# Optimization experiments

Hardware: AMD Instinct MI355X
Metric: run time of the kernel (lower is better)

Reference implementation:

```python
import jax
import jax.numpy as jnp
import numpy as np

B, S, D, H, HID, E, TOPK = 1, 2048, 1024, 16, 4096, 8, 2
HEAD_DIM = D // H


def _layer_norm(x, g, b, eps=1e-5):
    mu = jnp.mean(x, axis=-1, keepdims=True)
    var = jnp.var(x, axis=-1, keepdims=True)
    return (x - mu) * jax.lax.rsqrt(var + eps) * g + b


def setup_inputs() -> dict:
    key = jax.random.key(0)
    ks = jax.random.split(key, 12)
    s = 0.02
    return {
        "x": jax.random.normal(ks[0], (B, S, D), jnp.float32),
        "ln1_g": jnp.ones((D,), jnp.float32),
        "ln1_b": jnp.zeros((D,), jnp.float32),
        "wq": jax.random.normal(ks[1], (D, D), jnp.float32) * s,
        "wk": jax.random.normal(ks[2], (D, D), jnp.float32) * s,
        "wv": jax.random.normal(ks[3], (D, D), jnp.float32) * s,
        "wo": jax.random.normal(ks[4], (D, D), jnp.float32) * s,
        "ln2_g": jnp.ones((D,), jnp.float32),
        "ln2_b": jnp.zeros((D,), jnp.float32),
        "w_gate": jax.random.normal(ks[5], (D, E), jnp.float32) * s,
        "w_eg": jax.random.normal(ks[6], (E, D, HID), jnp.float32) * s,
        "w_eu": jax.random.normal(ks[7], (E, D, HID), jnp.float32) * s,
        "w_ed": jax.random.normal(ks[8], (E, HID, D), jnp.float32) * s,
    }


def _attention(h, wq, wk, wv, wo):
    b, s, d = h.shape
    q = (h @ wq).reshape(b, s, H, HEAD_DIM).transpose(0, 2, 1, 3)
    k = (h @ wk).reshape(b, s, H, HEAD_DIM).transpose(0, 2, 1, 3)
    v = (h @ wv).reshape(b, s, H, HEAD_DIM).transpose(0, 2, 1, 3)
    scores = jnp.einsum("bhqd,bhkd->bhqk", q, k) / jnp.sqrt(jnp.asarray(HEAD_DIM, h.dtype))
    causal = jnp.tril(jnp.ones((s, s), bool))  # [s,s]
    scores = jnp.where(causal, scores, jnp.asarray(-1e30, h.dtype))
    attn = jax.nn.softmax(scores, axis=-1)
    out = jnp.einsum("bhqk,bhkd->bhqd", attn, v).transpose(0, 2, 1, 3).reshape(b, s, d)
    return out @ wo


def _moe(h, w_gate, w_eg, w_eu, w_ed):
    b, s, d = h.shape
    flat = h.reshape(-1, d)  # [T,D]
    logits = flat @ w_gate  # [T,E]
    scores = jax.nn.sigmoid(logits)
    top_val, top_idx = jax.lax.top_k(scores, TOPK)
    top_val = top_val / (jnp.sum(top_val, axis=-1, keepdims=True) + 1e-9)
    # per-token per-expert combine weight (0 for unrouted experts)
    combine = jnp.sum(jax.nn.one_hot(top_idx, E, dtype=flat.dtype) * top_val[..., None], axis=1)  # [T,E]
    g = jax.nn.silu(jnp.einsum("td,edh->eth", flat, w_eg))
    u = jnp.einsum("td,edh->eth", flat, w_eu)
    eo = jnp.einsum("eth,ehd->etd", g * u, w_ed)  # [E,T,D]
    out = jnp.einsum("etd,te->td", eo, combine)
    return out.reshape(b, s, d)


def reference(x, ln1_g, ln1_b, wq, wk, wv, wo, ln2_g, ln2_b, w_gate, w_eg, w_eu, w_ed):
    x = x + _attention(_layer_norm(x, ln1_g, ln1_b), wq, wk, wv, wo)
    x = x + _moe(_layer_norm(x, ln2_g, ln2_b), w_gate, w_eg, w_eu, w_ed)
    return x
```

## Files before the change

kernel.cpp:

```cpp
#include <hip/hip_runtime.h>
#include <hip/hip_bf16.h>
#include <stdint.h>

#define DI __device__ __forceinline__

typedef short bf16x8_t __attribute__((ext_vector_type(8)));
typedef float f32x4_t __attribute__((ext_vector_type(4)));

DI unsigned short f2bf(float f) {
  __hip_bfloat16 h = __float2bfloat16(f);
  unsigned short u;
  __builtin_memcpy(&u, &h, 2);
  return u;
}

DI uint32_t pk2(float a, float b) {
  return (uint32_t)f2bf(a) | ((uint32_t)f2bf(b) << 16);
}

DI f32x4_t mfma16(bf16x8_t a, bf16x8_t b, f32x4_t c) {
  return __builtin_amdgcn_mfma_f32_16x16x32_bf16(a, b, c, 0, 0, 0);
}

DI void gload16(const void* g, void* l) {
  __builtin_amdgcn_global_load_lds(
      (const __attribute__((address_space(1))) uint32_t*)g,
      (__attribute__((address_space(3))) uint32_t*)l, 16, 0, 0);
}

DI bf16x8_t frag(const unsigned short* base, int row, int hi) {
  return *(const bf16x8_t*)&base[row * 32 + ((hi ^ ((row >> 1) & 3)) * 8)];
}
DI int chunk_swz(int tid) { return ((tid & 3) ^ ((tid >> 3) & 3)) * 8; }

__global__ __launch_bounds__(256) void transpose_cvt(const float* __restrict__ in,
                                                     unsigned short* __restrict__ out,
                                                     int R, int C) {
  __shared__ float tile[64][65];
  const int tid = threadIdx.x;
  const int tx = tid & 15, ty = tid >> 4;
  const size_t zoff = (size_t)blockIdx.z * R * C;
  const int r0 = blockIdx.y * 64, c0 = blockIdx.x * 64;
#pragma unroll
  for (int i = 0; i < 4; ++i) {
    const int r = ty + i * 16;
    const float4 v = *(const float4*)(in + zoff + (size_t)(r0 + r) * C + c0 + tx * 4);
    tile[r][tx * 4 + 0] = v.x; tile[r][tx * 4 + 1] = v.y;
    tile[r][tx * 4 + 2] = v.z; tile[r][tx * 4 + 3] = v.w;
  }
  __syncthreads();
#pragma unroll
  for (int i = 0; i < 4; ++i) {
    const int r = ty + i * 16;
    ushort4 o;
    o.x = f2bf(tile[tx * 4 + 0][r]); o.y = f2bf(tile[tx * 4 + 1][r]);
    o.z = f2bf(tile[tx * 4 + 2][r]); o.w = f2bf(tile[tx * 4 + 3][r]);
    *(ushort4*)(out + zoff + (size_t)(c0 + r) * R + r0 + tx * 4) = o;
  }
}

__global__ __launch_bounds__(256) void ln_kernel(const float* __restrict__ x, const float* __restrict__ g,
                                                 const float* __restrict__ b, unsigned short* __restrict__ out) {
  const int row = blockIdx.x, tid = threadIdx.x;
  const int wid = tid >> 6, lane = tid & 63;
  const float4 v = *(const float4*)(x + (size_t)row * 1024 + tid * 4);
  float s = v.x + v.y + v.z + v.w;
  float s2 = v.x * v.x + v.y * v.y + v.z * v.z + v.w * v.w;
#pragma unroll
  for (int o = 1; o < 64; o <<= 1) { s += __shfl_xor(s, o); s2 += __shfl_xor(s2, o); }
  __shared__ float red[8];
  if (lane == 0) { red[wid] = s; red[4 + wid] = s2; }
  __syncthreads();
  const float ts = red[0] + red[1] + red[2] + red[3];
  const float ts2 = red[4] + red[5] + red[6] + red[7];
  const float mu = ts * 0.0009765625f;
  const float var = ts2 * 0.0009765625f - mu * mu;
  const float rs = rsqrtf(var + 1e-5f);
  const float4 gg = *(const float4*)(g + tid * 4);
  const float4 bb = *(const float4*)(b + tid * 4);
  ushort4 o4;
  o4.x = f2bf((v.x - mu) * rs * gg.x + bb.x);
  o4.y = f2bf((v.y - mu) * rs * gg.y + bb.y);
  o4.z = f2bf((v.z - mu) * rs * gg.z + bb.z);
  o4.w = f2bf((v.w - mu) * rs * gg.w + bb.w);
  *(ushort4*)(out + (size_t)row * 1024 + tid * 4) = o4;
}

template<int BN>
DI void gemm_loop(const unsigned short* aR0, const unsigned short* aR1,
                  const unsigned short* bR0, const unsigned short* bR1,
                  const int K, unsigned short* lds, const int tid,
                  f32x4_t (&acc)[4][BN / 32]) {
  constexpr int NF = BN / 32;
  unsigned short* ldsA = lds;
  unsigned short* ldsB = lds + 4096;
  const int wid = tid >> 6, lane = tid & 63, ln = lane & 15, hi = lane >> 4;
  const int wr = wid >> 1, wc = wid & 1;
  char* dstA0 = (char*)ldsA + wid * 1024;
  char* dstA1 = (char*)ldsA + 4096 + wid * 1024;
  char* dstB0 = (char*)ldsB + wid * 1024;
  char* dstB1 = (char*)ldsB + 4096 + wid * 1024;
  for (int k0 = 0; k0 < K; k0 += 32) {
    gload16(aR0 + k0, dstA0);
    gload16(aR1 + k0, dstA1);
    gload16(bR0 + k0, dstB0);
    if constexpr (BN == 128) gload16(bR1 + k0, dstB1);
    __syncthreads();
    bf16x8_t af[4];
#pragma unroll
    for (int mf = 0; mf < 4; ++mf)
      af[mf] = frag(ldsA, wr * 64 + mf * 16 + ln, hi);
#pragma unroll
    for (int nf = 0; nf < NF; ++nf) {
      bf16x8_t bfr = frag(ldsB, wc * (BN / 2) + nf * 16 + ln, hi);
#pragma unroll
      for (int mf = 0; mf < 4; ++mf)
        acc[mf][nf] = mfma16(af[mf], bfr, acc[mf][nf]);
    }
    __syncthreads();
  }
}

__global__ __launch_bounds__(256) void qkv_kernel(const unsigned short* __restrict__ h1,
                                                  const unsigned short* __restrict__ wqT,
                                                  const unsigned short* __restrict__ wkT,
                                                  const unsigned short* __restrict__ wvT,
                                                  unsigned short* __restrict__ qb,
                                                  unsigned short* __restrict__ kbf,
                                                  unsigned short* __restrict__ vt) {
  __shared__ unsigned short lds[128 * 32 + 128 * 32];
  const int tid = threadIdx.x;
  const int z = blockIdx.z;
  const unsigned short* BT = (z == 0) ? wqT : (z == 1) ? wkT : wvT;
  const int m0 = blockIdx.y * 128, n0 = blockIdx.x * 128;
  f32x4_t acc[4][4] = {};
  const int cs = chunk_swz(tid);
  const unsigned short* aR0 = h1 + (size_t)(m0 + (tid >> 2)) * 1024 + cs;
  const unsigned short* aR1 = aR0 + 64 * 1024;
  const unsigned short* bR0 = BT + (size_t)(n0 + (tid >> 2)) * 1024 + cs;
  const unsigned short* bR1 = bR0 + 64 * 1024;
  gemm_loop<128>(aR0, aR1, bR0, bR1, 1024, lds, tid, acc);
  const int lane = tid & 63, ln = lane & 15, hi = lane >> 4, wid = tid >> 6;
  const int wr = wid >> 1, wc = wid & 1;
  if (z < 2) {
    unsigned short* o = z ? kbf : qb;
#pragma unroll
    for (int mf = 0; mf < 4; ++mf)
#pragma unroll
      for (int nf = 0; nf < 4; ++nf)
#pragma unroll
        for (int r = 0; r < 4; ++r) {
          const int m = m0 + wr * 64 + mf * 16 + hi * 4 + r;
          const int n = n0 + wc * 64 + nf * 16 + ln;
          o[(size_t)m * 1024 + n] = f2bf(acc[mf][nf][r]);
        }
  } else {
#pragma unroll
    for (int mf = 0; mf < 4; ++mf)
#pragma unroll
      for (int nf = 0; nf < 4; ++nf) {
        const int n = n0 + wc * 64 + nf * 16 + ln;
        const int mb = m0 + wr * 64 + mf * 16 + hi * 4;
        ushort4 o;
        o.x = f2bf(acc[mf][nf][0]); o.y = f2bf(acc[mf][nf][1]);
        o.z = f2bf(acc[mf][nf][2]); o.w = f2bf(acc[mf][nf][3]);
        *(ushort4*)(vt + (size_t)n * 2048 + mb) = o;
      }
  }
}

__global__ __launch_bounds__(256) void wo_kernel(const unsigned short* __restrict__ ao,
                                                 const unsigned short* __restrict__ woT,
                                                 const float* __restrict__ x,
                                                 float* __restrict__ out) {
  __shared__ unsigned short lds[128 * 32 + 64 * 32];
  const int tid = threadIdx.x;
  const int m0 = blockIdx.y * 128, n0 = blockIdx.x * 64;
  f32x4_t acc[4][2] = {};
  const int cs = chunk_swz(tid);
  const unsigned short* aR0 = ao + (size_t)(m0 + (tid >> 2)) * 1024 + cs;
  const unsigned short* aR1 = aR0 + 64 * 1024;
  const unsigned short* bR0 = woT + (size_t)(n0 + (tid >> 2)) * 1024 + cs;
  gemm_loop<64>(aR0, aR1, bR0, nullptr, 1024, lds, tid, acc);
  const int lane = tid & 63, ln = lane & 15, hi = lane >> 4, wid = tid >> 6;
  const int wr = wid >> 1, wc = wid & 1;
#pragma unroll
  for (int mf = 0; mf < 4; ++mf)
#pragma unroll
    for (int nf = 0; nf < 2; ++nf)
#pragma unroll
      for (int r = 0; r < 4; ++r) {
        const int m = m0 + wr * 64 + mf * 16 + hi * 4 + r;
        const int n = n0 + wc * 32 + nf * 16 + ln;
        out[(size_t)m * 1024 + n] = acc[mf][nf][r] + x[(size_t)m * 1024 + n];
      }
}

__global__ __launch_bounds__(256) void attn_kernel(const unsigned short* __restrict__ qb,
                                                   const unsigned short* __restrict__ kbuf,
                                                   const unsigned short* __restrict__ vt,
                                                   unsigned short* __restrict__ ao) {
  __shared__ unsigned short kTl[4096];
  __shared__ unsigned short vTl[4096];
  __shared__ unsigned short pl[4][1024];
  const int tid = threadIdx.x;
  const int wid = tid >> 6, lane = tid & 63;
  const int ln = lane & 15, hi = lane >> 4;
  const int h = blockIdx.y;
  const int q0 = blockIdx.x * 64;
  const int q0w = q0 + wid * 16;

  const unsigned short* qrow = qb + (size_t)(q0w + ln) * 1024 + h * 64 + hi * 8;
  const bf16x8_t aq0 = *(const bf16x8_t*)(qrow);
  const bf16x8_t aq1 = *(const bf16x8_t*)(qrow + 32);

  const int str_r = tid >> 3, str_c = tid & 7;
  const int swc = (str_c ^ (str_r & 7)) * 8;
  const unsigned short* ksrc0 = kbuf + (size_t)str_r * 1024 + h * 64 + swc;
  const unsigned short* ksrc1 = kbuf + (size_t)(str_r + 32) * 1024 + h * 64 + swc;
  const unsigned short* vsrc0 = vt + (size_t)(h * 64 + str_r) * 2048 + swc;
  const unsigned short* vsrc1 = vt + (size_t)(h * 64 + str_r + 32) * 2048 + swc;
  char* kd0 = (char*)kTl + wid * 1024;
  char* kd1 = (char*)kTl + 4096 + wid * 1024;
  char* vd0 = (char*)vTl + wid * 1024;
  char* vd1 = (char*)vTl + 4096 + wid * 1024;

  float m_r[4], l_r[4];
  f32x4_t o_acc[4] = {};
#pragma unroll
  for (int r = 0; r < 4; ++r) { m_r[r] = -1e30f; l_r[r] = 0.f; }

  const int nkv = blockIdx.x + 1;
  for (int it = 0; it < nkv; ++it) {
    const int kv0 = it * 64;
    gload16(ksrc0 + (size_t)kv0 * 1024, kd0);
    gload16(ksrc1 + (size_t)kv0 * 1024, kd1);
    gload16(vsrc0 + kv0, vd0);
    gload16(vsrc1 + kv0, vd1);
    __syncthreads();

    float sc[4][4];
#pragma unroll
    for (int cf = 0; cf < 4; ++cf) {
      const int row = cf * 16 + ln;
      const int swz = row & 7;
      const bf16x8_t b0 = *(const bf16x8_t*)((char*)kTl + row * 128 + ((hi ^ swz) * 16));
      const bf16x8_t b1 = *(const bf16x8_t*)((char*)kTl + row * 128 + (((4 + hi) ^ swz) * 16));
      f32x4_t zacc = {};
      zacc = mfma16(aq0, b0, zacc);
      zacc = mfma16(aq1, b1, zacc);
#pragma unroll
      for (int r = 0; r < 4; ++r) sc[cf][r] = zacc[r] * 0.125f;
    }
    if (kv0 + 63 > q0w) {
#pragma unroll
      for (int cf = 0; cf < 4; ++cf)
#pragma unroll
        for (int r = 0; r < 4; ++r) {
          const int qg = q0w + hi * 4 + r;
          const int kg = kv0 + cf * 16 + ln;
          if (kg > qg) sc[cf][r] = -1e30f;
        }
    }
#pragma unroll
    for (int r = 0; r < 4; ++r) {
      float tm = fmaxf(fmaxf(sc[0][r], sc[1][r]), fmaxf(sc[2][r], sc[3][r]));
      tm = fmaxf(tm, __shfl_xor(tm, 1));
      tm = fmaxf(tm, __shfl_xor(tm, 2));
      tm = fmaxf(tm, __shfl_xor(tm, 4));
      tm = fmaxf(tm, __shfl_xor(tm, 8));
      const float mn = fmaxf(m_r[r], tm);
      const float alpha = __expf(m_r[r] - mn);
      float rsum = 0.f;
#pragma unroll
      for (int cf = 0; cf < 4; ++cf) {
        const float p = __expf(sc[cf][r] - mn);
        sc[cf][r] = p; rsum += p;
      }
      rsum += __shfl_xor(rsum, 1); rsum += __shfl_xor(rsum, 2);
      rsum += __shfl_xor(rsum, 4); rsum += __shfl_xor(rsum, 8);
      l_r[r] = l_r[r] * alpha + rsum;
      m_r[r] = mn;
#pragma unroll
      for (int df = 0; df < 4; ++df) o_acc[df][r] *= alpha;
    }
    unsigned short* pw = &pl[wid][0];
#pragma unroll
    for (int cf = 0; cf < 4; ++cf)
#pragma unroll
      for (int r = 0; r < 4; ++r) {
        const int qq = hi * 4 + r;
        const int kv = cf * 16 + ln;
        const int bo = (qq * 128 + kv * 2) ^ ((qq & 7) << 4);
        *(unsigned short*)((char*)pw + bo) = f2bf(sc[cf][r]);
      }
    __syncthreads();
    const bf16x8_t pa0 = *(const bf16x8_t*)((char*)pw + ((ln * 128 + hi * 16) ^ ((ln & 7) << 4)));
    const bf16x8_t pa1 = *(const bf16x8_t*)((char*)pw + ((ln * 128 + 64 + hi * 16) ^ ((ln & 7) << 4)));
#pragma unroll
    for (int df = 0; df < 4; ++df) {
      const int d = df * 16 + ln;
      const int swz = d & 7;
      const bf16x8_t bv0 = *(const bf16x8_t*)((char*)vTl + d * 128 + ((hi ^ swz) * 16));
      const bf16x8_t bv1 = *(const bf16x8_t*)((char*)vTl + d * 128 + (((4 + hi) ^ swz) * 16));
      o_acc[df] = mfma16(pa0, bv0, o_acc[df]);
      o_acc[df] = mfma16(pa1, bv1, o_acc[df]);
    }
    __syncthreads();
  }
#pragma unroll
  for (int df = 0; df < 4; ++df) {
    const int n = h * 64 + df * 16 + ln;
#pragma unroll
    for (int r = 0; r < 4; ++r) {
      const int m = q0w + hi * 4 + r;
      ao[(size_t)m * 1024 + n] = f2bf(o_acc[df][r] / l_r[r]);
    }
  }
}

__global__ __launch_bounds__(256) void gate_kernel(const float* __restrict__ x2, const float* __restrict__ g,
                                                   const float* __restrict__ b, const float* __restrict__ wg,
                                                   int2* __restrict__ te, float2* __restrict__ tw,
                                                   int* __restrict__ cnt) {
  const int tid = threadIdx.x, wid = tid >> 6, lane = tid & 63;
  const int t = blockIdx.x * 4 + wid;
  const float* row = x2 + (size_t)t * 1024;
  float vv[16];
#pragma unroll
  for (int i = 0; i < 4; ++i) *(float4*)&vv[i * 4] = *(const float4*)(row + lane * 16 + i * 4);
  float s = 0.f, s2 = 0.f;
#pragma unroll
  for (int j = 0; j < 16; ++j) { s += vv[j]; s2 += vv[j] * vv[j]; }
#pragma unroll
  for (int o = 1; o < 64; o <<= 1) { s += __shfl_xor(s, o); s2 += __shfl_xor(s2, o); }
  const float mu = s * 0.0009765625f;
  const float var = s2 * 0.0009765625f - mu * mu;
  const float rs = rsqrtf(var + 1e-5f);
  float acc[8] = {0.f, 0.f, 0.f, 0.f, 0.f, 0.f, 0.f, 0.f};
#pragma unroll
  for (int j = 0; j < 16; ++j) {
    const int d = lane * 16 + j;
    const float xv = (vv[j] - mu) * rs * g[d] + b[d];
    const float4 w0 = *(const float4*)(wg + d * 8);
    const float4 w1 = *(const float4*)(wg + d * 8 + 4);
    acc[0] += xv * w0.x; acc[1] += xv * w0.y; acc[2] += xv * w0.z; acc[3] += xv * w0.w;
    acc[4] += xv * w1.x; acc[5] += xv * w1.y; acc[6] += xv * w1.z; acc[7] += xv * w1.w;
  }
#pragma unroll
  for (int o = 1; o < 64; o <<= 1) {
#pragma unroll
    for (int e = 0; e < 8; ++e) acc[e] += __shfl_xor(acc[e], o);
  }
  if (lane == 0) {
    float sg[8];
#pragma unroll
    for (int e = 0; e < 8; ++e) sg[e] = 1.f / (1.f + __expf(-acc[e]));
    int e0 = 0;
#pragma unroll
    for (int e = 1; e < 8; ++e) if (sg[e] > sg[e0]) e0 = e;
    int e1 = (e0 == 0) ? 1 : 0;
#pragma unroll
    for (int e = 0; e < 8; ++e) if (e != e0 && sg[e] > sg[e1]) e1 = e;
    const float v0 = sg[e0], v1 = sg[e1];
    const float inv = 1.f / (v0 + v1 + 1e-9f);
    te[t] = make_int2(e0, e1);
    tw[t] = make_float2(v0 * inv, v1 * inv);
    atomicAdd(&cnt[e0], 1);
    atomicAdd(&cnt[e1], 1);
  }
}

__global__ void zero_counters(int* p) { if (threadIdx.x < 8) p[threadIdx.x] = 0; }

__global__ void g2_kernel(const int* __restrict__ cnt, int* __restrict__ slot_off,
                          int* __restrict__ tile_expert, int* __restrict__ tile_rowbase,
                          int* __restrict__ cursor, int* __restrict__ assign_token,
                          float* __restrict__ assign_w) {
  const int tid = threadIdx.x;
  for (int i = tid; i < 5120; i += 64) { assign_token[i] = -1; assign_w[i] = 0.f; }
  if (tid == 0) {
    int base = 0, tiles = 0;
    for (int e = 0; e < 8; ++e) {
      const int c = cnt[e];
      slot_off[e] = base;
      cursor[e] = 0;
      const int nt = (c + 127) >> 7;
      for (int i = 0; i < nt; ++i) {
        tile_expert[tiles] = e;
        tile_rowbase[tiles] = base + i * 128;
        ++tiles;
      }
      base += nt * 128;
    }
    for (; tiles < 40; ++tiles) tile_expert[tiles] = -1;
  }
}

__global__ __launch_bounds__(256) void g3_kernel(const int2* __restrict__ te, const float2* __restrict__ tw,
                                                 const int* __restrict__ slot_off, int* __restrict__ cursor,
                                                 int* __restrict__ assign_token, float* __restrict__ assign_w) {
  const int t = blockIdx.x * 256 + threadIdx.x;
  const int2 e = te[t];
  const float2 w = tw[t];
  const int s0 = slot_off[e.x] + atomicAdd(&cursor[e.x], 1);
  assign_token[s0] = t; assign_w[s0] = w.x;
  const int s1 = slot_off[e.y] + atomicAdd(&cursor[e.y], 1);
  assign_token[s1] = t; assign_w[s1] = w.y;
}

__global__ __launch_bounds__(256) void upgate_kernel(const unsigned short* __restrict__ h2,
                                                     const float* __restrict__ w_eg, const float* __restrict__ w_eu,
                                                     const int* __restrict__ tile_expert,
                                                     const int* __restrict__ tile_rowbase,
                                                     const int* __restrict__ assign_token,
                                                     unsigned short* __restrict__ act) {
  const int by = blockIdx.y;
  const int e = tile_expert[by];
  if (e < 0) return;
  const int n0 = blockIdx.x * 64;
  const int rowbase = tile_rowbase[by];
  const int tid = threadIdx.x;
  __shared__ unsigned short lds[2 * 4096 + 2 * 4096];
  unsigned short* ldsA = lds;
  unsigned short* ldsB = lds + 8192;
  const int wid = tid >> 6, lane = tid & 63, ln = lane & 15, hi = lane >> 4;
  const int wr = wid >> 1, wc = wid & 1;
  const int r0s = rowbase + (tid >> 2);
  int t0 = assign_token[r0s];       t0 = t0 < 0 ? 0 : t0;
  int t1 = assign_token[r0s + 64];  t1 = t1 < 0 ? 0 : t1;
  const int cs = chunk_swz(tid);
  const unsigned short* aR0 = h2 + (size_t)t0 * 1024 + cs;
  const unsigned short* aR1 = h2 + (size_t)t1 * 1024 + cs;
  const int mat = tid >> 7;
  const int blk = tid & 127;
  const int kb = (blk >> 4) * 4;
  const int nb = (blk & 15) * 4;
  const float* bsrc = (mat ? w_eu : w_eg) + (size_t)e * 1024 * 4096 + (size_t)kb * 4096 + n0 + nb;
  int boff[4];
#pragma unroll
  for (int i = 0; i < 4; ++i) {
    const int n = nb + i;
    int bo = mat * 4096 + n * 64 + kb * 2;
    bo ^= ((n >> 2) & 7) << 4;
    boff[i] = bo;
  }
  f32x4_t accg[4][2] = {};
  f32x4_t accu[4][2] = {};
  {
    const float4 q0 = *(const float4*)(bsrc);
    const float4 q1 = *(const float4*)(bsrc + 4096);
    const float4 q2 = *(const float4*)(bsrc + 8192);
    const float4 q3 = *(const float4*)(bsrc + 12288);
    gload16(aR0, (char*)ldsA + wid * 1024);
    gload16(aR1, (char*)ldsA + 4096 + wid * 1024);
    const float* q0p = (const float*)&q0; const float* q1p = (const float*)&q1;
    const float* q2p = (const float*)&q2; const float* q3p = (const float*)&q3;
#pragma unroll
    for (int i = 0; i < 4; ++i) {
      uint2 w;
      w.x = pk2(q0p[i], q1p[i]);
      w.y = pk2(q2p[i], q3p[i]);
      *(uint2*)((char*)ldsB + boff[i]) = w;
    }
  }
  asm volatile("s_waitcnt lgkmcnt(0)" ::: "memory");
  __builtin_amdgcn_sched_barrier(0);
  __builtin_amdgcn_s_barrier();
  int buf = 0;
  for (int it = 0; it < 31; ++it) {
    const int kn = (it + 1) * 32;
    const int nbuf = buf ^ 1;
    const float* bs = bsrc + (size_t)kn * 4096;
    const float4 q0 = *(const float4*)(bs);
    const float4 q1 = *(const float4*)(bs + 4096);
    const float4 q2 = *(const float4*)(bs + 8192);
    const float4 q3 = *(const float4*)(bs + 12288);
    gload16(aR0 + kn, (char*)ldsA + nbuf * 8192 + wid * 1024);
    gload16(aR1 + kn, (char*)ldsA + nbuf * 8192 + 4096 + wid * 1024);
    asm volatile("s_waitcnt vmcnt(6)" ::: "memory");
    __builtin_amdgcn_sched_barrier(0);
    const unsigned short* A = ldsA + buf * 4096;
    const char* Bb = (char*)ldsB + buf * 8192;
    bf16x8_t af[4];
#pragma unroll
    for (int mf = 0; mf < 4; ++mf)
      af[mf] = frag(A, wr * 64 + mf * 16 + ln, hi);
#pragma unroll
    for (int nf = 0; nf < 2; ++nf) {
      const int nrow = wc * 32 + nf * 16 + ln;
      int bo = nrow * 64 + hi * 16;
      bo ^= ((nrow >> 2) & 7) << 4;
      const bf16x8_t bg = *(const bf16x8_t*)(Bb + bo);
      const bf16x8_t bu = *(const bf16x8_t*)(Bb + 4096 + bo);
#pragma unroll
      for (int mf = 0; mf < 4; ++mf) {
        accg[mf][nf] = mfma16(af[mf], bg, accg[mf][nf]);
        accu[mf][nf] = mfma16(af[mf], bu, accu[mf][nf]);
      }
    }
    {
      char* Bn = (char*)ldsB + nbuf * 8192;
      const float* q0p = (const float*)&q0; const float* q1p = (const float*)&q1;
      const float* q2p = (const float*)&q2; const float* q3p = (const float*)&q3;
#pragma unroll
      for (int i = 0; i < 4; ++i) {
        uint2 w;
        w.x = pk2(q0p[i], q1p[i]);
        w.y = pk2(q2p[i], q3p[i]);
        *(uint2*)(Bn + boff[i]) = w;
      }
    }
    asm volatile("s_waitcnt lgkmcnt(0)" ::: "memory");
    __builtin_amdgcn_sched_barrier(0);
    __builtin_amdgcn_s_barrier();
    buf = nbuf;
  }
  asm volatile("s_waitcnt vmcnt(0)" ::: "memory");
  __builtin_amdgcn_sched_barrier(0);
  {
    const unsigned short* A = ldsA + buf * 4096;
    const char* Bb = (char*)ldsB + buf * 8192;
    bf16x8_t af[4];
#pragma unroll
    for (int mf = 0; mf < 4; ++mf)
      af[mf] = frag(A, wr * 64 + mf * 16 + ln, hi);
#pragma unroll
    for (int nf = 0; nf < 2; ++nf) {
      const int nrow = wc * 32 + nf * 16 + ln;
      int bo = nrow * 64 + hi * 16;
      bo ^= ((nrow >> 2) & 7) << 4;
      const bf16x8_t bg = *(const bf16x8_t*)(Bb + bo);
      const bf16x8_t bu = *(const bf16x8_t*)(Bb + 4096 + bo);
#pragma unroll
      for (int mf = 0; mf < 4; ++mf) {
        accg[mf][nf] = mfma16(af[mf], bg, accg[mf][nf]);
        accu[mf][nf] = mfma16(af[mf], bu, accu[mf][nf]);
      }
    }
  }
#pragma unroll
  for (int mf = 0; mf < 4; ++mf)
#pragma unroll
    for (int nf = 0; nf < 2; ++nf)
#pragma unroll
      for (int r = 0; r < 4; ++r) {
        const int m = wr * 64 + mf * 16 + hi * 4 + r;
        const int n = n0 + wc * 32 + nf * 16 + ln;
        const float gv = accg[mf][nf][r], uv = accu[mf][nf][r];
        const float val = gv / (1.f + __expf(-gv)) * uv;
        act[(size_t)(rowbase + m) * 4096 + n] = f2bf(val);
      }
}

__global__ __launch_bounds__(256) void down_kernel(const unsigned short* __restrict__ act,
                                                   const float* __restrict__ w_ed,
                                                   const int* __restrict__ tile_expert,
                                                   const int* __restrict__ tile_rowbase,
                                                   const int* __restrict__ assign_token,
                                                   const float* __restrict__ assign_w,
                                                   float* __restrict__ out) {
  const int by = blockIdx.y;
  const int e = tile_expert[by];
  if (e < 0) return;
  const int n0 = blockIdx.x * 64;
  const int rowbase = tile_rowbase[by];
  const int tid = threadIdx.x;
  __shared__ unsigned short lds[2 * 4096 + 2 * 2048];
  unsigned short* ldsA = lds;
  unsigned short* ldsB = lds + 8192;
  const int wid = tid >> 6, lane = tid & 63, ln = lane & 15, hi = lane >> 4;
  const int wr = wid >> 1, wc = wid & 1;
  const int cs = chunk_swz(tid);
  const unsigned short* aR0 = act + (size_t)(rowbase + (tid >> 2)) * 4096 + cs;
  const unsigned short* aR1 = aR0 + (size_t)64 * 4096;
  const int nb = (tid & 15) * 4;
  const int kb2 = (tid >> 4) * 2;
  const float* bsrc = w_ed + (size_t)e * 4096 * 1024 + (size_t)kb2 * 1024 + n0 + nb;
  int boff[4];
#pragma unroll
  for (int i = 0; i < 4; ++i) {
    const int n = nb + i;
    int bo = n * 64 + kb2 * 2;
    bo ^= ((n >> 2) & 7) << 4;
    boff[i] = bo;
  }
  f32x4_t acc[4][2] = {};
  {
    const float4 q0 = *(const float4*)(bsrc);
    const float4 q1 = *(const float4*)(bsrc + 1024);
    gload16(aR0, (char*)ldsA + wid * 1024);
    gload16(aR1, (char*)ldsA + 4096 + wid * 1024);
    const float* q0p = (const float*)&q0; const float* q1p = (const float*)&q1;
#pragma unroll
    for (int i = 0; i < 4; ++i)
      *(uint32_t*)((char*)ldsB + boff[i]) = pk2(q0p[i], q1p[i]);
  }
  asm volatile("s_waitcnt lgkmcnt(0)" ::: "memory");
  __builtin_amdgcn_sched_barrier(0);
  __builtin_amdgcn_s_barrier();
  int buf = 0;
  for (int it = 0; it < 127; ++it) {
    const int kn = (it + 1) * 32;
    const int nbuf = buf ^ 1;
    const float* bs = bsrc + (size_t)kn * 1024;
    const float4 q0 = *(const float4*)(bs);
    const float4 q1 = *(const float4*)(bs + 1024);
    gload16(aR0 + kn, (char*)ldsA + nbuf * 8192 + wid * 1024);
    gload16(aR1 + kn, (char*)ldsA + nbuf * 8192 + 4096 + wid * 1024);
    asm volatile("s_waitcnt vmcnt(4)" ::: "memory");
    __builtin_amdgcn_sched_barrier(0);
    const unsigned short* A = ldsA + buf * 4096;
    const char* Bb = (char*)ldsB + buf * 4096;
    bf16x8_t af[4];
#pragma unroll
    for (int mf = 0; mf < 4; ++mf)
      af[mf] = frag(A, wr * 64 + mf * 16 + ln, hi);
#pragma unroll
    for (int nf = 0; nf < 2; ++nf) {
      const int nrow = wc * 32 + nf * 16 + ln;
      int bo = nrow * 64 + hi * 16;
      bo ^= ((nrow >> 2) & 7) << 4;
      const bf16x8_t bb = *(const bf16x8_t*)(Bb + bo);
#pragma unroll
      for (int mf = 0; mf < 4; ++mf)
        acc[mf][nf] = mfma16(af[mf], bb, acc[mf][nf]);
    }
    {
      char* Bn = (char*)ldsB + nbuf * 4096;
      const float* q0p = (const float*)&q0; const float* q1p = (const float*)&q1;
#pragma unroll
      for (int i = 0; i < 4; ++i)
        *(uint32_t*)(Bn + boff[i]) = pk2(q0p[i], q1p[i]);
    }
    asm volatile("s_waitcnt lgkmcnt(0)" ::: "memory");
    __builtin_amdgcn_sched_barrier(0);
    __builtin_amdgcn_s_barrier();
    buf = nbuf;
  }
  asm volatile("s_waitcnt vmcnt(0)" ::: "memory");
  __builtin_amdgcn_sched_barrier(0);
  {
    const unsigned short* A = ldsA + buf * 4096;
    const char* Bb = (char*)ldsB + buf * 4096;
    bf16x8_t af[4];
#pragma unroll
    for (int mf = 0; mf < 4; ++mf)
      af[mf] = frag(A, wr * 64 + mf * 16 + ln, hi);
#pragma unroll
    for (int nf = 0; nf < 2; ++nf) {
      const int nrow = wc * 32 + nf * 16 + ln;
      int bo = nrow * 64 + hi * 16;
      bo ^= ((nrow >> 2) & 7) << 4;
      const bf16x8_t bb = *(const bf16x8_t*)(Bb + bo);
#pragma unroll
      for (int mf = 0; mf < 4; ++mf)
        acc[mf][nf] = mfma16(af[mf], bb, acc[mf][nf]);
    }
  }
#pragma unroll
  for (int mf = 0; mf < 4; ++mf)
#pragma unroll
    for (int r = 0; r < 4; ++r) {
      const int m = wr * 64 + mf * 16 + hi * 4 + r;
      const int slot = rowbase + m;
      const int tk = assign_token[slot];
      if (tk >= 0) {
        const float w = assign_w[slot];
#pragma unroll
        for (int nf = 0; nf < 2; ++nf) {
          const int n = n0 + wc * 32 + nf * 16 + ln;
          atomicAdd(out + (size_t)tk * 1024 + n, acc[mf][nf][r] * w);
        }
      }
    }
}

extern "C" void kernel_launch(void* const* d_in, const int* in_sizes, int n_in,
                              void* d_out, int out_size, void* d_ws, size_t ws_size,
                              hipStream_t stream) {
  (void)in_sizes; (void)n_in; (void)out_size;
  const float* x    = (const float*)d_in[0];
  const float* ln1g = (const float*)d_in[1];
  const float* ln1b = (const float*)d_in[2];
  const float* wq   = (const float*)d_in[3];
  const float* wk   = (const float*)d_in[4];
  const float* wv   = (const float*)d_in[5];
  const float* wo   = (const float*)d_in[6];
  const float* ln2g = (const float*)d_in[7];
  const float* ln2b = (const float*)d_in[8];
  const float* wg   = (const float*)d_in[9];
  const float* weg  = (const float*)d_in[10];
  const float* weu  = (const float*)d_in[11];
  const float* wed  = (const float*)d_in[12];
  float* out = (float*)d_out;
  char* ws = (char*)d_ws;

  const size_t MB = (size_t)1 << 20;
  if (ws_size < 74 * MB) return;
  unsigned short* wqT = (unsigned short*)(ws + 0 * MB);
  unsigned short* wkT = (unsigned short*)(ws + 2 * MB);
  unsigned short* wvT = (unsigned short*)(ws + 4 * MB);
  unsigned short* woT = (unsigned short*)(ws + 6 * MB);
  unsigned short* h1  = (unsigned short*)(ws + 8 * MB);
  unsigned short* qb  = (unsigned short*)(ws + 12 * MB);
  unsigned short* kbf = (unsigned short*)(ws + 16 * MB);
  unsigned short* vt  = (unsigned short*)(ws + 20 * MB);
  unsigned short* ao  = (unsigned short*)(ws + 24 * MB);
  unsigned short* h2  = (unsigned short*)(ws + 28 * MB);
  unsigned short* act = (unsigned short*)(ws + 32 * MB);
  int2*   te = (int2*)(ws + 72 * MB);
  float2* tw = (float2*)(ws + 72 * MB + 16384);
  int*  meta = (int*)(ws + 72 * MB + 32768);
  int* cnt = meta;
  int* cursor = meta + 8;
  int* slot_off = meta + 16;
  int* tile_expert = meta + 24;
  int* tile_rowbase = meta + 64;
  int*   assign_token = (int*)(ws + 72 * MB + 36864);
  float* assign_w     = (float*)(ws + 72 * MB + 36864 + 20480);

  zero_counters<<<1, 64, 0, stream>>>(cnt);
  transpose_cvt<<<dim3(16, 16, 1), 256, 0, stream>>>(wq, wqT, 1024, 1024);
  transpose_cvt<<<dim3(16, 16, 1), 256, 0, stream>>>(wk, wkT, 1024, 1024);
  transpose_cvt<<<dim3(16, 16, 1), 256, 0, stream>>>(wv, wvT, 1024, 1024);
  transpose_cvt<<<dim3(16, 16, 1), 256, 0, stream>>>(wo, woT, 1024, 1024);
  ln_kernel<<<2048, 256, 0, stream>>>(x, ln1g, ln1b, h1);
  qkv_kernel<<<dim3(8, 16, 3), 256, 0, stream>>>(h1, wqT, wkT, wvT, qb, kbf, vt);
  attn_kernel<<<dim3(32, 16), 256, 0, stream>>>(qb, kbf, vt, ao);
  wo_kernel<<<dim3(16, 16), 256, 0, stream>>>(ao, woT, x, out);
  ln_kernel<<<2048, 256, 0, stream>>>(out, ln2g, ln2b, h2);
  gate_kernel<<<512, 256, 0, stream>>>(out, ln2g, ln2b, wg, te, tw, cnt);
  g2_kernel<<<1, 64, 0, stream>>>(cnt, slot_off, tile_expert, tile_rowbase, cursor, assign_token, assign_w);
  g3_kernel<<<8, 256, 0, stream>>>(te, tw, slot_off, cursor, assign_token, assign_w);
  upgate_kernel<<<dim3(64, 40), 256, 0, stream>>>(h2, weg, weu, tile_expert, tile_rowbase, assign_token, act);
  down_kernel<<<dim3(16, 40), 256, 0, stream>>>(act, wed, tile_expert, tile_rowbase, assign_token, assign_w, out);
}
```

Baseline: 498.9 us.

## Enlarge MoE expert tiles to 256 rows with explicit ping-pong pipelining

Doubles the per-block M tile in the expert up/gate and down GEMMs from 128 to 256 token slots, so each fp32 weight tile loaded and converted to bf16 is reused across twice as many tokens. The k-loop is restructured into unrolled ping-pong stages with B fragments held in registers a stage ahead. Routing metadata is rebuilt for 256-row tiles and the workspace is enlarged. The cost is more register pressure from 8x2 accumulators, more LDS per block, and more padding waste per expert with a smaller grid.

```diff
diff --git a/kernel.cpp b/kernel.cpp
--- a/kernel.cpp
+++ b/kernel.cpp
@@ -373,25 +373,25 @@
 
 __global__ void zero_counters(int* p) { if (threadIdx.x < 8) p[threadIdx.x] = 0; }
 
-__global__ void g2_kernel(const int* __restrict__ cnt, int* __restrict__ slot_off,
-                          int* __restrict__ tile_expert, int* __restrict__ tile_rowbase,
-                          int* __restrict__ cursor, int* __restrict__ assign_token,
-                          float* __restrict__ assign_w) {
+__global__ __launch_bounds__(256) void g2_kernel(const int* __restrict__ cnt, int* __restrict__ slot_off,
+                                                 int* __restrict__ tile_expert, int* __restrict__ tile_rowbase,
+                                                 int* __restrict__ cursor, int* __restrict__ assign_token,
+                                                 float* __restrict__ assign_w) {
   const int tid = threadIdx.x;
-  for (int i = tid; i < 5120; i += 64) { assign_token[i] = -1; assign_w[i] = 0.f; }
+  for (int i = tid; i < 8192; i += 256) { assign_token[i] = -1; assign_w[i] = 0.f; }
   if (tid == 0) {
     int base = 0, tiles = 0;
     for (int e = 0; e < 8; ++e) {
       const int c = cnt[e];
       slot_off[e] = base;
       cursor[e] = 0;
-      const int nt = (c + 127) >> 7;
+      const int nt = (c + 255) >> 8;
       for (int i = 0; i < nt; ++i) {
         tile_expert[tiles] = e;
-        tile_rowbase[tiles] = base + i * 128;
+        tile_rowbase[tiles] = base + i * 256;
         ++tiles;
       }
-      base += nt * 128;
+      base += nt * 256;
     }
     for (; tiles < 40; ++tiles) tile_expert[tiles] = -1;
   }
@@ -409,29 +409,78 @@
   assign_token[s1] = t; assign_w[s1] = w.y;
 }
 
-__global__ __launch_bounds__(256) void upgate_kernel(const unsigned short* __restrict__ h2,
-                                                     const float* __restrict__ w_eg, const float* __restrict__ w_eu,
-                                                     const int* __restrict__ tile_expert,
-                                                     const int* __restrict__ tile_rowbase,
-                                                     const int* __restrict__ assign_token,
-                                                     unsigned short* __restrict__ act) {
+DI void stageA4(const unsigned short* a0, const unsigned short* a1,
+                const unsigned short* a2, const unsigned short* a3,
+                int koff, char* Ab, int wid) {
+  gload16(a0 + koff, Ab + wid * 1024);
+  gload16(a1 + koff, Ab + 4096 + wid * 1024);
+  gload16(a2 + koff, Ab + 8192 + wid * 1024);
+  gload16(a3 + koff, Ab + 12288 + wid * 1024);
+}
+
+DI void ug_write_b(char* Bn, const int* boff, const float4& q0, const float4& q1,
+                   const float4& q2, const float4& q3) {
+  const float* q0p = (const float*)&q0; const float* q1p = (const float*)&q1;
+  const float* q2p = (const float*)&q2; const float* q3p = (const float*)&q3;
+#pragma unroll
+  for (int i = 0; i < 4; ++i) {
+    uint2 w;
+    w.x = pk2(q0p[i], q1p[i]);
+    w.y = pk2(q2p[i], q3p[i]);
+    *(uint2*)(Bn + boff[i]) = w;
+  }
+}
+
+DI void ug_mfma256(const unsigned short* A, const char* Bb, int wr, int wc, int ln, int hi,
+                   f32x4_t (&accg)[8][2], f32x4_t (&accu)[8][2]) {
+  bf16x8_t af[8];
+#pragma unroll
+  for (int mf = 0; mf < 8; ++mf)
+    af[mf] = frag(A, wr * 128 + mf * 16 + ln, hi);
+#pragma unroll
+  for (int nf = 0; nf < 2; ++nf) {
+    const int nrow = wc * 32 + nf * 16 + ln;
+    int bo = nrow * 64 + hi * 16;
+    bo ^= ((nrow >> 2) & 7) << 4;
+    const bf16x8_t bg = *(const bf16x8_t*)(Bb + bo);
+    const bf16x8_t bu = *(const bf16x8_t*)(Bb + 4096 + bo);
+#pragma unroll
+    for (int mf = 0; mf < 8; ++mf) {
+      accg[mf][nf] = mfma16(af[mf], bg, accg[mf][nf]);
+      accu[mf][nf] = mfma16(af[mf], bu, accu[mf][nf]);
+    }
+  }
+}
+
+__global__ __launch_bounds__(256, 2) void upgate_kernel(const unsigned short* __restrict__ h2,
+                                                        const float* __restrict__ w_eg, const float* __restrict__ w_eu,
+                                                        const int* __restrict__ tile_expert,
+                                                        const int* __restrict__ tile_rowbase,
+                                                        const int* __restrict__ assign_token,
+                                                        unsigned short* __restrict__ act) {
   const int by = blockIdx.y;
   const int e = tile_expert[by];
   if (e < 0) return;
   const int n0 = blockIdx.x * 64;
   const int rowbase = tile_rowbase[by];
   const int tid = threadIdx.x;
-  __shared__ unsigned short lds[2 * 4096 + 2 * 4096];
-  unsigned short* ldsA = lds;
-  unsigned short* ldsB = lds + 8192;
+  __shared__ unsigned short lds[2 * 8192 + 2 * 4096];
+  char* A0 = (char*)lds;
+  char* A1 = (char*)lds + 16384;
+  char* B0 = (char*)lds + 32768;
+  char* B1 = (char*)lds + 40960;
   const int wid = tid >> 6, lane = tid & 63, ln = lane & 15, hi = lane >> 4;
   const int wr = wid >> 1, wc = wid & 1;
   const int r0s = rowbase + (tid >> 2);
-  int t0 = assign_token[r0s];       t0 = t0 < 0 ? 0 : t0;
-  int t1 = assign_token[r0s + 64];  t1 = t1 < 0 ? 0 : t1;
+  int tk0 = assign_token[r0s];        tk0 = tk0 < 0 ? 0 : tk0;
+  int tk1 = assign_token[r0s + 64];   tk1 = tk1 < 0 ? 0 : tk1;
+  int tk2 = assign_token[r0s + 128];  tk2 = tk2 < 0 ? 0 : tk2;
+  int tk3 = assign_token[r0s + 192];  tk3 = tk3 < 0 ? 0 : tk3;
   const int cs = chunk_swz(tid);
-  const unsigned short* aR0 = h2 + (size_t)t0 * 1024 + cs;
-  const unsigned short* aR1 = h2 + (size_t)t1 * 1024 + cs;
+  const unsigned short* aR0 = h2 + (size_t)tk0 * 1024 + cs;
+  const unsigned short* aR1 = h2 + (size_t)tk1 * 1024 + cs;
+  const unsigned short* aR2 = h2 + (size_t)tk2 * 1024 + cs;
+  const unsigned short* aR3 = h2 + (size_t)tk3 * 1024 + cs;
   const int mat = tid >> 7;
   const int blk = tid & 127;
   const int kb = (blk >> 4) * 4;
@@ -445,107 +494,82 @@
     bo ^= ((n >> 2) & 7) << 4;
     boff[i] = bo;
   }
-  f32x4_t accg[4][2] = {};
-  f32x4_t accu[4][2] = {};
+  f32x4_t accg[8][2] = {};
+  f32x4_t accu[8][2] = {};
+  float4 qA0, qA1, qA2, qA3, qB0, qB1, qB2, qB3;
+  qB0 = *(const float4*)(bsrc);
+  qB1 = *(const float4*)(bsrc + 4096);
+  qB2 = *(const float4*)(bsrc + 8192);
+  qB3 = *(const float4*)(bsrc + 12288);
+  stageA4(aR0, aR1, aR2, aR3, 0, A0, wid);
+  __builtin_amdgcn_sched_barrier(0);
+  ug_write_b(B0, boff, qB0, qB1, qB2, qB3);
   {
-    const float4 q0 = *(const float4*)(bsrc);
-    const float4 q1 = *(const float4*)(bsrc + 4096);
-    const float4 q2 = *(const float4*)(bsrc + 8192);
-    const float4 q3 = *(const float4*)(bsrc + 12288);
-    gload16(aR0, (char*)ldsA + wid * 1024);
-    gload16(aR1, (char*)ldsA + 4096 + wid * 1024);
-    const float* q0p = (const float*)&q0; const float* q1p = (const float*)&q1;
-    const float* q2p = (const float*)&q2; const float* q3p = (const float*)&q3;
-#pragma unroll
-    for (int i = 0; i < 4; ++i) {
-      uint2 w;
-      w.x = pk2(q0p[i], q1p[i]);
-      w.y = pk2(q2p[i], q3p[i]);
-      *(uint2*)((char*)ldsB + boff[i]) = w;
-    }
-  }
+    const float* bs = bsrc + (size_t)32 * 4096;
+    qA0 = *(const float4*)(bs);
+    qA1 = *(const float4*)(bs + 4096);
+    qA2 = *(const float4*)(bs + 8192);
+    qA3 = *(const float4*)(bs + 12288);
+  }
+  stageA4(aR0, aR1, aR2, aR3, 32, A1, wid);
+  asm volatile("s_waitcnt vmcnt(8)" ::: "memory");
+  __builtin_amdgcn_sched_barrier(0);
   asm volatile("s_waitcnt lgkmcnt(0)" ::: "memory");
   __builtin_amdgcn_sched_barrier(0);
   __builtin_amdgcn_s_barrier();
-  int buf = 0;
-  for (int it = 0; it < 31; ++it) {
-    const int kn = (it + 1) * 32;
-    const int nbuf = buf ^ 1;
-    const float* bs = bsrc + (size_t)kn * 4096;
-    const float4 q0 = *(const float4*)(bs);
-    const float4 q1 = *(const float4*)(bs + 4096);
-    const float4 q2 = *(const float4*)(bs + 8192);
-    const float4 q3 = *(const float4*)(bs + 12288);
-    gload16(aR0 + kn, (char*)ldsA + nbuf * 8192 + wid * 1024);
-    gload16(aR1 + kn, (char*)ldsA + nbuf * 8192 + 4096 + wid * 1024);
-    asm volatile("s_waitcnt vmcnt(6)" ::: "memory");
-    __builtin_amdgcn_sched_barrier(0);
-    const unsigned short* A = ldsA + buf * 4096;
-    const char* Bb = (char*)ldsB + buf * 8192;
-    bf16x8_t af[4];
-#pragma unroll
-    for (int mf = 0; mf < 4; ++mf)
-      af[mf] = frag(A, wr * 64 + mf * 16 + ln, hi);
-#pragma unroll
-    for (int nf = 0; nf < 2; ++nf) {
-      const int nrow = wc * 32 + nf * 16 + ln;
-      int bo = nrow * 64 + hi * 16;
-      bo ^= ((nrow >> 2) & 7) << 4;
-      const bf16x8_t bg = *(const bf16x8_t*)(Bb + bo);
-      const bf16x8_t bu = *(const bf16x8_t*)(Bb + 4096 + bo);
-#pragma unroll
-      for (int mf = 0; mf < 4; ++mf) {
-        accg[mf][nf] = mfma16(af[mf], bg, accg[mf][nf]);
-        accu[mf][nf] = mfma16(af[mf], bu, accu[mf][nf]);
-      }
-    }
+  for (int p = 0; p < 15; ++p) {
     {
-      char* Bn = (char*)ldsB + nbuf * 8192;
-      const float* q0p = (const float*)&q0; const float* q1p = (const float*)&q1;
-      const float* q2p = (const float*)&q2; const float* q3p = (const float*)&q3;
-#pragma unroll
-      for (int i = 0; i < 4; ++i) {
-        uint2 w;
-        w.x = pk2(q0p[i], q1p[i]);
-        w.y = pk2(q2p[i], q3p[i]);
-        *(uint2*)(Bn + boff[i]) = w;
-      }
-    }
-    asm volatile("s_waitcnt lgkmcnt(0)" ::: "memory");
-    __builtin_amdgcn_sched_barrier(0);
-    __builtin_amdgcn_s_barrier();
-    buf = nbuf;
-  }
+      const int t = 2 * p;
+      const float* bs = bsrc + (size_t)(t + 2) * 32 * 4096;
+      qB0 = *(const float4*)(bs);
+      qB1 = *(const float4*)(bs + 4096);
+      qB2 = *(const float4*)(bs + 8192);
+      qB3 = *(const float4*)(bs + 12288);
+      stageA4(aR0, aR1, aR2, aR3, (t + 1) * 32, A1, wid);
+      __builtin_amdgcn_sched_barrier(0);
+      ug_write_b(B1, boff, qA0, qA1, qA2, qA3);
+      ug_mfma256((const unsigned short*)A0, B0, wr, wc, ln, hi, accg, accu);
+      asm volatile("s_waitcnt vmcnt(4)" ::: "memory");
+      __builtin_amdgcn_sched_barrier(0);
+      asm volatile("s_waitcnt lgkmcnt(0)" ::: "memory");
+      __builtin_amdgcn_sched_barrier(0);
+      __builtin_amdgcn_s_barrier();
+    }
+    {
+      const int t = 2 * p + 1;
+      const float* bs = bsrc + (size_t)(t + 2) * 32 * 4096;
+      qA0 = *(const float4*)(bs);
+      qA1 = *(const float4*)(bs + 4096);
+      qA2 = *(const float4*)(bs + 8192);
+      qA3 = *(const float4*)(bs + 12288);
+      stageA4(aR0, aR1, aR2, aR3, (t + 1) * 32, A0, wid);
+      __builtin_amdgcn_sched_barrier(0);
+      ug_write_b(B0, boff, qB0, qB1, qB2, qB3);
+      ug_mfma256((const unsigned short*)A1, B1, wr, wc, ln, hi, accg, accu);
+      asm volatile("s_waitcnt vmcnt(4)" ::: "memory");
+      __builtin_amdgcn_sched_barrier(0);
+      asm volatile("s_waitcnt lgkmcnt(0)" ::: "memory");
+      __builtin_amdgcn_sched_barrier(0);
+      __builtin_amdgcn_s_barrier();
+    }
+  }
+  stageA4(aR0, aR1, aR2, aR3, 31 * 32, A1, wid);
+  __builtin_amdgcn_sched_barrier(0);
+  ug_write_b(B1, boff, qA0, qA1, qA2, qA3);
+  ug_mfma256((const unsigned short*)A0, B0, wr, wc, ln, hi, accg, accu);
   asm volatile("s_waitcnt vmcnt(0)" ::: "memory");
   __builtin_amdgcn_sched_barrier(0);
-  {
-    const unsigned short* A = ldsA + buf * 4096;
-    const char* Bb = (char*)ldsB + buf * 8192;
-    bf16x8_t af[4];
-#pragma unroll
-    for (int mf = 0; mf < 4; ++mf)
-      af[mf] = frag(A, wr * 64 + mf * 16 + ln, hi);
-#pragma unroll
-    for (int nf = 0; nf < 2; ++nf) {
-      const int nrow = wc * 32 + nf * 16 + ln;
-      int bo = nrow * 64 + hi * 16;
-      bo ^= ((nrow >> 2) & 7) << 4;
-      const bf16x8_t bg = *(const bf16x8_t*)(Bb + bo);
-      const bf16x8_t bu = *(const bf16x8_t*)(Bb + 4096 + bo);
-#pragma unroll
-      for (int mf = 0; mf < 4; ++mf) {
-        accg[mf][nf] = mfma16(af[mf], bg, accg[mf][nf]);
-        accu[mf][nf] = mfma16(af[mf], bu, accu[mf][nf]);
-      }
-    }
-  }
-#pragma unroll
-  for (int mf = 0; mf < 4; ++mf)
+  asm volatile("s_waitcnt lgkmcnt(0)" ::: "memory");
+  __builtin_amdgcn_sched_barrier(0);
+  __builtin_amdgcn_s_barrier();
+  ug_mfma256((const unsigned short*)A1, B1, wr, wc, ln, hi, accg, accu);
+#pragma unroll
+  for (int mf = 0; mf < 8; ++mf)
 #pragma unroll
     for (int nf = 0; nf < 2; ++nf)
 #pragma unroll
       for (int r = 0; r < 4; ++r) {
-        const int m = wr * 64 + mf * 16 + hi * 4 + r;
+        const int m = wr * 128 + mf * 16 + hi * 4 + r;
         const int n = n0 + wc * 32 + nf * 16 + ln;
         const float gv = accg[mf][nf][r], uv = accu[mf][nf][r];
         const float val = gv / (1.f + __expf(-gv)) * uv;
@@ -553,27 +577,56 @@
       }
 }
 
-__global__ __launch_bounds__(256) void down_kernel(const unsigned short* __restrict__ act,
-                                                   const float* __restrict__ w_ed,
-                                                   const int* __restrict__ tile_expert,
-                                                   const int* __restrict__ tile_rowbase,
-                                                   const int* __restrict__ assign_token,
-                                                   const float* __restrict__ assign_w,
-                                                   float* __restrict__ out) {
+DI void dn_write_b(char* Bn, const int* boff, const float4& q0, const float4& q1) {
+  const float* q0p = (const float*)&q0; const float* q1p = (const float*)&q1;
+#pragma unroll
+  for (int i = 0; i < 4; ++i)
+    *(uint32_t*)(Bn + boff[i]) = pk2(q0p[i], q1p[i]);
+}
+
+DI void dn_mfma256(const unsigned short* A, const char* Bb, int wr, int wc, int ln, int hi,
+                   f32x4_t (&acc)[8][2]) {
+  bf16x8_t af[8];
+#pragma unroll
+  for (int mf = 0; mf < 8; ++mf)
+    af[mf] = frag(A, wr * 128 + mf * 16 + ln, hi);
+#pragma unroll
+  for (int nf = 0; nf < 2; ++nf) {
+    const int nrow = wc * 32 + nf * 16 + ln;
+    int bo = nrow * 64 + hi * 16;
+    bo ^= ((nrow >> 2) & 7) << 4;
+    const bf16x8_t bb = *(const bf16x8_t*)(Bb + bo);
+#pragma unroll
+    for (int mf = 0; mf < 8; ++mf)
+      acc[mf][nf] = mfma16(af[mf], bb, acc[mf][nf]);
+  }
+}
+
+__global__ __launch_bounds__(256, 2) void down_kernel(const unsigned short* __restrict__ act,
+                                                      const float* __restrict__ w_ed,
+                                                      const int* __restrict__ tile_expert,
+                                                      const int* __restrict__ tile_rowbase,
+                                                      const int* __restrict__ assign_token,
+                                                      const float* __restrict__ assign_w,
+                                                      float* __restrict__ out) {
   const int by = blockIdx.y;
   const int e = tile_expert[by];
   if (e < 0) return;
   const int n0 = blockIdx.x * 64;
   const int rowbase = tile_rowbase[by];
   const int tid = threadIdx.x;
-  __shared__ unsigned short lds[2 * 4096 + 2 * 2048];
-  unsigned short* ldsA = lds;
-  unsigned short* ldsB = lds + 8192;
+  __shared__ unsigned short lds[2 * 8192 + 2 * 2048];
+  char* A0 = (char*)lds;
+  char* A1 = (char*)lds + 16384;
+  char* B0 = (char*)lds + 32768;
+  char* B1 = (char*)lds + 36864;
   const int wid = tid >> 6, lane = tid & 63, ln = lane & 15, hi = lane >> 4;
   const int wr = wid >> 1, wc = wid & 1;
   const int cs = chunk_swz(tid);
   const unsigned short* aR0 = act + (size_t)(rowbase + (tid >> 2)) * 4096 + cs;
   const unsigned short* aR1 = aR0 + (size_t)64 * 4096;
+  const unsigned short* aR2 = aR0 + (size_t)128 * 4096;
+  const unsigned short* aR3 = aR0 + (size_t)192 * 4096;
   const int nb = (tid & 15) * 4;
   const int kb2 = (tid >> 4) * 2;
   const float* bsrc = w_ed + (size_t)e * 4096 * 1024 + (size_t)kb2 * 1024 + n0 + nb;
@@ -585,84 +638,71 @@
     bo ^= ((n >> 2) & 7) << 4;
     boff[i] = bo;
   }
-  f32x4_t acc[4][2] = {};
+  f32x4_t acc[8][2] = {};
+  float4 qA0, qA1, qB0, qB1;
+  qB0 = *(const float4*)(bsrc);
+  qB1 = *(const float4*)(bsrc + 1024);
+  stageA4(aR0, aR1, aR2, aR3, 0, A0, wid);
+  __builtin_amdgcn_sched_barrier(0);
+  dn_write_b(B0, boff, qB0, qB1);
   {
-    const float4 q0 = *(const float4*)(bsrc);
-    const float4 q1 = *(const float4*)(bsrc + 1024);
-    gload16(aR0, (char*)ldsA + wid * 1024);
-    gload16(aR1, (char*)ldsA + 4096 + wid * 1024);
-    const float* q0p = (const float*)&q0; const float* q1p = (const float*)&q1;
-#pragma unroll
-    for (int i = 0; i < 4; ++i)
-      *(uint32_t*)((char*)ldsB + boff[i]) = pk2(q0p[i], q1p[i]);
-  }
+    const float* bs = bsrc + (size_t)32 * 1024;
+    qA0 = *(const float4*)(bs);
+    qA1 = *(const float4*)(bs + 1024);
+  }
+  stageA4(aR0, aR1, aR2, aR3, 32, A1, wid);
+  asm volatile("s_waitcnt vmcnt(6)" ::: "memory");
+  __builtin_amdgcn_sched_barrier(0);
   asm volatile("s_waitcnt lgkmcnt(0)" ::: "memory");
   __builtin_amdgcn_sched_barrier(0);
   __builtin_amdgcn_s_barrier();
-  int buf = 0;
-  for (int it = 0; it < 127; ++it) {
-    const int kn = (it + 1) * 32;
-    const int nbuf = buf ^ 1;
-    const float* bs = bsrc + (size_t)kn * 1024;
-    const float4 q0 = *(const float4*)(bs);
-    const float4 q1 = *(const float4*)(bs + 1024);
-    gload16(aR0 + kn, (char*)ldsA + nbuf * 8192 + wid * 1024);
-    gload16(aR1 + kn, (char*)ldsA + nbuf * 8192 + 4096 + wid * 1024);
-    asm volatile("s_waitcnt vmcnt(4)" ::: "memory");
-    __builtin_amdgcn_sched_barrier(0);
-    const unsigned short* A = ldsA + buf * 4096;
-    const char* Bb = (char*)ldsB + buf * 4096;
-    bf16x8_t af[4];
-#pragma unroll
-    for (int mf = 0; mf < 4; ++mf)
-      af[mf] = frag(A, wr * 64 + mf * 16 + ln, hi);
-#pragma unroll
-    for (int nf = 0; nf < 2; ++nf) {
-      const int nrow = wc * 32 + nf * 16 + ln;
-      int bo = nrow * 64 + hi * 16;
-      bo ^= ((nrow >> 2) & 7) << 4;
-      const bf16x8_t bb = *(const bf16x8_t*)(Bb + bo);
-#pragma unroll
-      for (int mf = 0; mf < 4; ++mf)
-        acc[mf][nf] = mfma16(af[mf], bb, acc[mf][nf]);
-    }
+  for (int p = 0; p < 63; ++p) {
     {
-      char* Bn = (char*)ldsB + nbuf * 4096;
-      const float* q0p = (const float*)&q0; const float* q1p = (const float*)&q1;
-#pragma unroll
-      for (int i = 0; i < 4; ++i)
-        *(uint32_t*)(Bn + boff[i]) = pk2(q0p[i], q1p[i]);
-    }
-    asm volatile("s_waitcnt lgkmcnt(0)" ::: "memory");
-    __builtin_amdgcn_sched_barrier(0);
-    __builtin_amdgcn_s_barrier();
-    buf = nbuf;
-  }
+      const int t = 2 * p;
+      const float* bs = bsrc + (size_t)(t + 2) * 32 * 1024;
+      qB0 = *(const float4*)(bs);
+      qB1 = *(const float4*)(bs + 1024);
+      stageA4(aR0, aR1, aR2, aR3, (t + 1) * 32, A1, wid);
+      __builtin_amdgcn_sched_barrier(0);
+      dn_write_b(B1, boff, qA0, qA1);
+      dn_mfma256((const unsigned short*)A0, B0, wr, wc, ln, hi, acc);
+      asm volatile("s_waitcnt vmcnt(2)" ::: "memory");
+      __builtin_amdgcn_sched_barrier(0);
+      asm volatile("s_waitcnt lgkmcnt(0)" ::: "memory");
+      __builtin_amdgcn_sched_barrier(0);
+      __builtin_amdgcn_s_barrier();
+    }
+    {
+      const int t = 2 * p + 1;
+      const float* bs = bsrc + (size_t)(t + 2) * 32 * 1024;
+      qA0 = *(const float4*)(bs);
+      qA1 = *(const float4*)(bs + 1024);
+      stageA4(aR0, aR1, aR2, aR3, (t + 1) * 32, A0, wid);
+      __builtin_amdgcn_sched_barrier(0);
+      dn_write_b(B0, boff, qB0, qB1);
+      dn_mfma256((const unsigned short*)A1, B1, wr, wc, ln, hi, acc);
+      asm volatile("s_waitcnt vmcnt(2)" ::: "memory");
+      __builtin_amdgcn_sched_barrier(0);
+      asm volatile("s_waitcnt lgkmcnt(0)" ::: "memory");
+      __builtin_amdgcn_sched_barrier(0);
+      __builtin_amdgcn_s_barrier();
+    }
+  }
+  stageA4(aR0, aR1, aR2, aR3, 127 * 32, A1, wid);
+  __builtin_amdgcn_sched_barrier(0);
+  dn_write_b(B1, boff, qA0, qA1);
+  dn_mfma256((const unsigned short*)A0, B0, wr, wc, ln, hi, acc);
   asm volatile("s_waitcnt vmcnt(0)" ::: "memory");
   __builtin_amdgcn_sched_barrier(0);
-  {
-    const unsigned short* A = ldsA + buf * 4096;
-    const char* Bb = (char*)ldsB + buf * 4096;
-    bf16x8_t af[4];
-#pragma unroll
-    for (int mf = 0; mf < 4; ++mf)
-      af[mf] = frag(A, wr * 64 + mf * 16 + ln, hi);
-#pragma unroll
-    for (int nf = 0; nf < 2; ++nf) {
-      const int nrow = wc * 32 + nf * 16 + ln;
-      int bo = nrow * 64 + hi * 16;
-      bo ^= ((nrow >> 2) & 7) << 4;
-      const bf16x8_t bb = *(const bf16x8_t*)(Bb + bo);
-#pragma unroll
-      for (int mf = 0; mf < 4; ++mf)
-        acc[mf][nf] = mfma16(af[mf], bb, acc[mf][nf]);
-    }
-  }
-#pragma unroll
-  for (int mf = 0; mf < 4; ++mf)
+  asm volatile("s_waitcnt lgkmcnt(0)" ::: "memory");
+  __builtin_amdgcn_sched_barrier(0);
+  __builtin_amdgcn_s_barrier();
+  dn_mfma256((const unsigned short*)A1, B1, wr, wc, ln, hi, acc);
+#pragma unroll
+  for (int mf = 0; mf < 8; ++mf)
 #pragma unroll
     for (int r = 0; r < 4; ++r) {
-      const int m = wr * 64 + mf * 16 + hi * 4 + r;
+      const int m = wr * 128 + mf * 16 + hi * 4 + r;
       const int slot = rowbase + m;
       const int tk = assign_token[slot];
       if (tk >= 0) {
@@ -697,7 +737,7 @@
   char* ws = (char*)d_ws;
 
   const size_t MB = (size_t)1 << 20;
-  if (ws_size < 74 * MB) return;
+  if (ws_size < 86 * MB) return;
   unsigned short* wqT = (unsigned short*)(ws + 0 * MB);
   unsigned short* wkT = (unsigned short*)(ws + 2 * MB);
   unsigned short* wvT = (unsigned short*)(ws + 4 * MB);
@@ -709,16 +749,16 @@
   unsigned short* ao  = (unsigned short*)(ws + 24 * MB);
   unsigned short* h2  = (unsigned short*)(ws + 28 * MB);
   unsigned short* act = (unsigned short*)(ws + 32 * MB);
-  int2*   te = (int2*)(ws + 72 * MB);
-  float2* tw = (float2*)(ws + 72 * MB + 16384);
-  int*  meta = (int*)(ws + 72 * MB + 32768);
+  int2*   te = (int2*)(ws + 84 * MB);
+  float2* tw = (float2*)(ws + 84 * MB + 16384);
+  int*  meta = (int*)(ws + 84 * MB + 32768);
   int* cnt = meta;
   int* cursor = meta + 8;
   int* slot_off = meta + 16;
   int* tile_expert = meta + 24;
   int* tile_rowbase = meta + 64;
-  int*   assign_token = (int*)(ws + 72 * MB + 36864);
-  float* assign_w     = (float*)(ws + 72 * MB + 36864 + 20480);
+  int*   assign_token = (int*)(ws + 84 * MB + 36864);
+  float* assign_w     = (float*)(ws + 84 * MB + 36864 + 32768);
 
   zero_counters<<<1, 64, 0, stream>>>(cnt);
   transpose_cvt<<<dim3(16, 16, 1), 256, 0, stream>>>(wq, wqT, 1024, 1024);
@@ -731,8 +771,8 @@
   wo_kernel<<<dim3(16, 16), 256, 0, stream>>>(ao, woT, x, out);
   ln_kernel<<<2048, 256, 0, stream>>>(out, ln2g, ln2b, h2);
   gate_kernel<<<512, 256, 0, stream>>>(out, ln2g, ln2b, wg, te, tw, cnt);
-  g2_kernel<<<1, 64, 0, stream>>>(cnt, slot_off, tile_expert, tile_rowbase, cursor, assign_token, assign_w);
+  g2_kernel<<<1, 256, 0, stream>>>(cnt, slot_off, tile_expert, tile_rowbase, cursor, assign_token, assign_w);
   g3_kernel<<<8, 256, 0, stream>>>(te, tw, slot_off, cursor, assign_token, assign_w);
-  upgate_kernel<<<dim3(64, 40), 256, 0, stream>>>(h2, weg, weu, tile_expert, tile_rowbase, assign_token, act);
-  down_kernel<<<dim3(16, 40), 256, 0, stream>>>(act, wed, tile_expert, tile_rowbase, assign_token, assign_w, out);
-}
+  upgate_kernel<<<dim3(64, 24), 256, 0, stream>>>(h2, weg, weu, tile_expert, tile_rowbase, assign_token, act);
+  down_kernel<<<dim3(16, 24), 256, 0, stream>>>(act, wed, tile_expert, tile_rowbase, assign_token, assign_w, out);
+}
```

Measured after the change: 524.7 us. +5.2%, slower.
